# Kernel tuning notes

Measured on AMD Instinct MI355X. Metric: run time of the kernel, lower is better.

Reference implementation:

```python
import jax, jax.numpy as jnp
import numpy as np

B, L, D, N = 8, 512, 768, 64
H = 4 * D  # projection-layer expansion (create_projection_layer: d -> 4d -> out)


def _mlp(x, W1, b1, W2, b2):
    # Linear -> ReLU -> (Dropout, identity in eval) -> Linear
    return jax.nn.relu(x @ W1 + b1) @ W2 + b2


def setup_inputs() -> dict:
    key = jax.random.key(0)
    ks = jax.random.split(key, 18)
    s = 0.02
    inp = {
        "h": jax.random.normal(ks[0], (B, L, D), dtype=jnp.float32),
        "span_idx": jax.random.randint(ks[1], (B, N, 2), 0, L, dtype=jnp.int64),
        # project_start: D -> 4D -> D
        "Ws1": jax.random.normal(ks[2], (D, H), dtype=jnp.float32) * s,
        "bs1": jnp.zeros((H,), jnp.float32),
        "Ws2": jax.random.normal(ks[3], (H, D), dtype=jnp.float32) * s,
        "bs2": jnp.zeros((D,), jnp.float32),
        # project_end: D -> 4D -> D
        "We1": jax.random.normal(ks[4], (D, H), dtype=jnp.float32) * s,
        "be1": jnp.zeros((H,), jnp.float32),
        "We2": jax.random.normal(ks[5], (H, D), dtype=jnp.float32) * s,
        "be2": jnp.zeros((D,), jnp.float32),
        # span_marker.out_project: 2D -> 8D -> D (in=2D so hidden=4*2D? No: create_projection_layer(hidden*2,...)->Linear(2D,4*... ) uses 2D->8D? Faithful: Linear(in, in*4)->Linear(in*4,out) => 2D->8D->D
        "Wo1": jax.random.normal(ks[6], (2 * D, 8 * D), dtype=jnp.float32) * s,
        "bo1": jnp.zeros((8 * D,), jnp.float32),
        "Wo2": jax.random.normal(ks[7], (8 * D, D), dtype=jnp.float32) * s,
        "bo2": jnp.zeros((D,), jnp.float32),
        # rel out_project: 2D -> 8D -> D
        "Wr1": jax.random.normal(ks[8], (2 * D, 8 * D), dtype=jnp.float32) * s,
        "br1": jnp.zeros((8 * D,), jnp.float32),
        "Wr2": jax.random.normal(ks[9], (8 * D, D), dtype=jnp.float32) * s,
        "br2": jnp.zeros((D,), jnp.float32),
    }
    return inp


def reference(h, span_idx, Ws1, bs1, Ws2, bs2, We1, be1, We2, be2,
              Wo1, bo1, Wo2, bo2, Wr1, br1, Wr2, br2):
    Bn, Ln, Dn = h.shape
    Nn = span_idx.shape[1]
    batch_ix = jnp.arange(Bn)[:, None]  # [B,1]

    start_rep = _mlp(h, Ws1, bs1, Ws2, bs2)  # [B,L,D]
    end_rep = _mlp(h, We1, be1, We2, be2)    # [B,L,D]

    # extract_elements: gather span start/end token reps
    start_span = start_rep[batch_ix, span_idx[:, :, 0]]  # [B,N,D]
    end_span = end_rep[batch_ix, span_idx[:, :, 1]]      # [B,N,D]

    cat = jax.nn.relu(jnp.concatenate([start_span, end_span], axis=-1))  # [B,N,2D]
    entity_reps = _mlp(cat, Wo1, bo1, Wo2, bo2)  # [B,N,D]

    # all off-diagonal ordered pairs (i, j), i != j, row-major (matches torch mask)
    ii, jj = np.meshgrid(np.arange(Nn), np.arange(Nn), indexing="ij")
    m = ii != jj
    idx_i = jnp.asarray(ii[m])  # [N*(N-1)]
    idx_j = jnp.asarray(jj[m])

    pairs = jnp.concatenate(
        [entity_reps[:, idx_i], entity_reps[:, idx_j]], axis=-1
    )  # [B, N*(N-1), 2D]

    return _mlp(pairs, Wr1, br1, Wr2, br2)  # [B, N*(N-1), D]
```

## Files before the change

kernel.cpp:

```cpp
#include <hip/hip_runtime.h>

typedef unsigned short u16;
typedef __attribute__((ext_vector_type(8))) short short8;
typedef __attribute__((ext_vector_type(4))) short short4v;
typedef __attribute__((ext_vector_type(4))) float f32x4;

#define DEVI static __device__ __forceinline__

DEVI u16 f2bf(float f) {
  unsigned u = __builtin_bit_cast(unsigned, f);
  u += 0x7FFFu + ((u >> 16) & 1u);
  return (u16)(u >> 16);
}

DEVI float bf2f(u16 x) {
  unsigned u = ((unsigned)x) << 16;
  return __builtin_bit_cast(float, u);
}

DEVI unsigned cvtpk(float lo, float hi) {
  unsigned r;
  asm("v_cvt_pk_bf16_f32 %0, %1, %2" : "=v"(r) : "v"(lo), "v"(hi));
  return r;
}

DEVI void glds16(const void* g, void* l) {
  __builtin_amdgcn_global_load_lds(
      (const __attribute__((address_space(1))) unsigned*)g,
      (__attribute__((address_space(3))) unsigned*)l, 16, 0, 0);
}

struct TSeg { const float* W; u16* WT; int K, N, tstart; };
struct TDesc { TSeg s[8]; };

__global__ void k_transpose_all(TDesc d) {
  __shared__ __align__(16) float t[64][68];
  int bx = blockIdx.x;
  int si = 0;
#pragma unroll
  for (int k = 1; k < 8; ++k) si = (bx >= d.s[k].tstart) ? k : si;
  const float* W = d.s[si].W;
  u16* WT = d.s[si].WT;
  int K = d.s[si].K, N = d.s[si].N;
  int local = bx - d.s[si].tstart;
  int tpr = N >> 6;
  int n0 = (local % tpr) << 6;
  int k0 = (local / tpr) << 6;
  int tx = threadIdx.x;
  int ty = threadIdx.y;
#pragma unroll
  for (int r = 0; r < 4; ++r) {
    float4 v = *(const float4*)(W + (size_t)(k0 + ty * 4 + r) * N + n0 + tx * 4);
    *(float4*)&t[ty * 4 + r][tx * 4] = v;
  }
  __syncthreads();
#pragma unroll
  for (int r = 0; r < 4; ++r) {
    int nr = ty * 4 + r;
    short4v o;
    o[0] = (short)f2bf(t[tx * 4 + 0][nr]);
    o[1] = (short)f2bf(t[tx * 4 + 1][nr]);
    o[2] = (short)f2bf(t[tx * 4 + 2][nr]);
    o[3] = (short)f2bf(t[tx * 4 + 3][nr]);
    *(short4v*)(WT + (size_t)(n0 + nr) * K + k0 + tx * 4) = o;
  }
}

__global__ void k_gather(const float* __restrict__ h,
                         const int* __restrict__ span,
                         u16* __restrict__ xs, u16* __restrict__ xe) {
  int row = blockIdx.x;
  int b = row >> 6;
  int s = span[row * 2 + 0];
  int e = span[row * 2 + 1];
  const float* hs = h + ((size_t)b * 512 + s) * 768;
  const float* he = h + ((size_t)b * 512 + e) * 768;
  for (int d = threadIdx.x; d < 768; d += 256) {
    xs[(size_t)row * 768 + d] = f2bf(hs[d]);
    xe[(size_t)row * 768 + d] = f2bf(he[d]);
  }
}

__global__ __launch_bounds__(256)
void k_gemm(const u16* __restrict__ A0, const u16* __restrict__ A1, int lda,
            const u16* __restrict__ B0, const u16* __restrict__ B1, int ldb,
            const float* __restrict__ bias0, const float* __restrict__ bias1,
            void* __restrict__ C0, void* __restrict__ C1, int ldc,
            int kLen, int mtiles, int nsplit, int flags) {
  __shared__ __align__(16) u16 As[128 * 64];
  __shared__ __align__(16) u16 Bs[128 * 64];
  int z = blockIdx.z;
  int g = z / nsplit, c = z - g * nsplit;
  const u16* A = (g ? A1 : A0) + c * kLen;
  const u16* BT = (g ? B1 : B0) + c * kLen;
  const float* bias = g ? bias1 : bias0;
  void* C = g ? C1 : C0;

  int tid = threadIdx.x;
  int lane = tid & 63;
  int wave = tid >> 6;
  int wr = (wave >> 1) * 64, wc = (wave & 1) * 64;
  int bx = blockIdx.x;
  int m0 = (bx % mtiles) * 128;
  int n0 = (bx / mtiles) * 128;
  const int lr = lane & 15, hi = lane >> 4;

  f32x4 acc[4][4] = {};

  for (int k0 = 0; k0 < kLen; k0 += 64) {
#pragma unroll
    for (int it = 0; it < 4; ++it) {
      int s = it * 256 + tid;
      int row = s >> 3, gg = s & 7;
      int gc = (gg ^ (row & 7)) * 8;
      glds16(A + (size_t)(m0 + row) * lda + k0 + gc, (char*)As + s * 16);
      glds16(BT + (size_t)(n0 + row) * ldb + k0 + gc, (char*)Bs + s * 16);
    }
    __syncthreads();
#pragma unroll
    for (int kk = 0; kk < 2; ++kk) {
      short8 af[4], bf[4];
      int gk = kk * 4 + hi;
#pragma unroll
      for (int m = 0; m < 4; ++m) {
        int row = wr + m * 16 + lr;
        af[m] = *(const short8*)((const char*)As + row * 128 + ((gk ^ (row & 7)) * 16));
      }
#pragma unroll
      for (int n = 0; n < 4; ++n) {
        int row = wc + n * 16 + lr;
        bf[n] = *(const short8*)((const char*)Bs + row * 128 + ((gk ^ (row & 7)) * 16));
      }
#pragma unroll
      for (int m = 0; m < 4; ++m)
#pragma unroll
        for (int n = 0; n < 4; ++n)
          acc[m][n] = __builtin_amdgcn_mfma_f32_16x16x32_bf16(af[m], bf[n], acc[m][n], 0, 0, 0);
    }
    __syncthreads();
  }

  if (flags & 4) {
    float* P = (float*)C + (size_t)c * (mtiles * 128) * ldc;
#pragma unroll
    for (int n = 0; n < 4; ++n) {
      int col = n0 + wc + n * 16 + lr;
#pragma unroll
      for (int m = 0; m < 4; ++m)
#pragma unroll
        for (int r = 0; r < 4; ++r) {
          int row = m0 + wr + m * 16 + hi * 4 + r;
          P[(size_t)row * ldc + col] = acc[m][n][r];
        }
    }
  } else {
    bool relu = flags & 1;
#pragma unroll
    for (int n = 0; n < 4; ++n) {
      int col = n0 + wc + n * 16 + lr;
      float bv = bias ? bias[col] : 0.f;
#pragma unroll
      for (int m = 0; m < 4; ++m)
#pragma unroll
        for (int r = 0; r < 4; ++r) {
          int row = m0 + wr + m * 16 + hi * 4 + r;
          float v = acc[m][n][r] + bv;
          if (relu) v = fmaxf(v, 0.f);
          ((u16*)C)[(size_t)row * ldc + col] = f2bf(v);
        }
    }
  }
}

__global__ void k_fin_cat(const float* __restrict__ Ps, const float* __restrict__ Pe,
                          const float* __restrict__ b0, const float* __restrict__ b1,
                          u16* __restrict__ cat) {
  int t = blockIdx.x * 256 + threadIdx.x;
  int row = t / 384;
  int c4 = (t - row * 384) * 4;
  const float* P = Ps;
  const float* bias = b0;
  int lc = c4;
  if (c4 >= 768) { P = Pe; bias = b1; lc = c4 - 768; }
  f32x4 s = {};
#pragma unroll
  for (int ch = 0; ch < 4; ++ch)
    s += *(const f32x4*)(P + ((size_t)ch * 512 + row) * 768 + lc);
#pragma unroll
  for (int e = 0; e < 4; ++e)
    cat[(size_t)row * 1536 + c4 + e] = f2bf(fmaxf(s[e] + bias[lc + e], 0.f));
}

__global__ void k_fin_ent(const float* __restrict__ Po,
                          const float* __restrict__ bias,
                          u16* __restrict__ ent) {
  int t = blockIdx.x * 256 + threadIdx.x;
  int row = t / 192;
  int c4 = (t - row * 192) * 4;
  f32x4 s = {};
#pragma unroll
  for (int ch = 0; ch < 8; ++ch)
    s += *(const f32x4*)(Po + ((size_t)ch * 512 + row) * 768 + c4);
#pragma unroll
  for (int e = 0; e < 4; ++e)
    ent[(size_t)row * 768 + c4 + e] = f2bf(s[e] + bias[c4 + e]);
}

__global__ __launch_bounds__(512, 4)
void k_pair_gemm(const u16* __restrict__ U, const u16* __restrict__ V,
                 const u16* __restrict__ Wr2T,
                 const float* __restrict__ br2,
                 float* __restrict__ out) {
  __shared__ __align__(16) u16 As[128 * 64];
  __shared__ __align__(16) u16 Bs[2][256 * 64];
  int tid = threadIdx.x;
  int lane = tid & 63;
  int wave = tid >> 6;
  int wr = (wave >> 2) * 64;
  int wc = (wave & 3) * 64;
  const int lr = lane & 15, hi = lane >> 4;

  int nwg = gridDim.x;
  int orig = blockIdx.x;
  int xcd = orig & 7, rem = nwg & 7, qn = nwg >> 3;
  int wgid = (xcd < rem ? xcd * (qn + 1) : rem * (qn + 1) + (xcd - rem) * qn) + (orig >> 3);
  int mt = wgid % 252;
  int nt = wgid / 252;
  int m0 = mt * 128, n0 = nt * 256;

  int r = tid >> 2, q = tid & 3;
  int mrow = m0 + r;
  int b = mrow / 4032;
  int p = mrow - b * 4032;
  int i = p / 63;
  int j0 = p - i * 63;
  int j = j0 + (j0 >= i ? 1 : 0);
  const u16* uR = U + (size_t)(b * 64 + i) * 6144 + q * 16;
  const u16* vR = V + (size_t)(b * 64 + j) * 6144 + q * 16;
  char* aw0 = (char*)As + r * 128 + (((q * 2 + 0) ^ (r & 7)) * 16);
  char* aw1 = (char*)As + r * 128 + (((q * 2 + 1) ^ (r & 7)) * 16);

  f32x4 acc[4][4] = {};

  auto stageB = [&](int t, int buf) {
#pragma unroll
    for (int it = 0; it < 4; ++it) {
      int s = it * 512 + tid;
      int row = s >> 3, g = s & 7;
      int gc = (g ^ (row & 7)) * 8;
      glds16(Wr2T + (size_t)(n0 + row) * 6144 + t * 64 + gc,
             (char*)Bs[buf] + s * 16);
    }
  };

  stageB(0, 0);
  short8 ua = *(const short8*)(uR);
  short8 ub = *(const short8*)(uR + 8);
  short8 vva = *(const short8*)(vR);
  short8 vvb = *(const short8*)(vR + 8);

  for (int t = 0; t < 96; ++t) {
    unsigned w0[4], w1[4];
#pragma unroll
    for (int e = 0; e < 4; ++e) {
      float a0 = fmaxf(bf2f((u16)ua[2 * e])     + bf2f((u16)vva[2 * e]), 0.f);
      float a1 = fmaxf(bf2f((u16)ua[2 * e + 1]) + bf2f((u16)vva[2 * e + 1]), 0.f);
      w0[e] = cvtpk(a0, a1);
      float b0 = fmaxf(bf2f((u16)ub[2 * e])     + bf2f((u16)vvb[2 * e]), 0.f);
      float b1 = fmaxf(bf2f((u16)ub[2 * e + 1]) + bf2f((u16)vvb[2 * e + 1]), 0.f);
      w1[e] = cvtpk(b0, b1);
    }
    __syncthreads();
    *(uint4*)aw0 = *(uint4*)w0;
    *(uint4*)aw1 = *(uint4*)w1;
    if (t + 1 < 96) {
      ua  = *(const short8*)(uR + (t + 1) * 64);
      ub  = *(const short8*)(uR + (t + 1) * 64 + 8);
      vva = *(const short8*)(vR + (t + 1) * 64);
      vvb = *(const short8*)(vR + (t + 1) * 64 + 8);
      stageB(t + 1, (t + 1) & 1);
    }
    asm volatile("s_waitcnt lgkmcnt(0)\n\ts_barrier" ::: "memory");
    __builtin_amdgcn_sched_barrier(0);

    const u16* Bc = Bs[t & 1];
#pragma unroll
    for (int kk = 0; kk < 2; ++kk) {
      short8 af[4], bf[4];
      int gk = kk * 4 + hi;
#pragma unroll
      for (int m = 0; m < 4; ++m) {
        int row = wr + m * 16 + lr;
        af[m] = *(const short8*)((const char*)As + row * 128 + ((gk ^ (row & 7)) * 16));
      }
#pragma unroll
      for (int n = 0; n < 4; ++n) {
        int row = wc + n * 16 + lr;
        bf[n] = *(const short8*)((const char*)Bc + row * 128 + ((gk ^ (row & 7)) * 16));
      }
#pragma unroll
      for (int m = 0; m < 4; ++m)
#pragma unroll
        for (int n = 0; n < 4; ++n)
          acc[m][n] = __builtin_amdgcn_mfma_f32_16x16x32_bf16(af[m], bf[n], acc[m][n], 0, 0, 0);
    }
  }

#pragma unroll
  for (int n = 0; n < 4; ++n) {
    int col = n0 + wc + n * 16 + lr;
    float bv = br2[col];
#pragma unroll
    for (int m = 0; m < 4; ++m)
#pragma unroll
      for (int rg = 0; rg < 4; ++rg) {
        int row = m0 + wr + m * 16 + hi * 4 + rg;
        out[(size_t)row * 768 + col] = acc[m][n][rg] + bv;
      }
  }
}

constexpr size_t OFF_Ws1T = 0;
constexpr size_t OFF_Ws2T = OFF_Ws1T + (size_t)3072 * 768 * 2;
constexpr size_t OFF_We1T = OFF_Ws2T + (size_t)768 * 3072 * 2;
constexpr size_t OFF_We2T = OFF_We1T + (size_t)3072 * 768 * 2;
constexpr size_t OFF_Wo1T = OFF_We2T + (size_t)768 * 3072 * 2;
constexpr size_t OFF_Wo2T = OFF_Wo1T + (size_t)6144 * 1536 * 2;
constexpr size_t OFF_Wr1T = OFF_Wo2T + (size_t)768 * 6144 * 2;
constexpr size_t OFF_Wr2T = OFF_Wr1T + (size_t)6144 * 1536 * 2;
constexpr size_t OFF_XS   = OFF_Wr2T + (size_t)768 * 6144 * 2;
constexpr size_t OFF_XE   = OFF_XS + (size_t)512 * 768 * 2;
constexpr size_t OFF_HS1  = OFF_XE + (size_t)512 * 768 * 2;
constexpr size_t OFF_HE1  = OFF_HS1 + (size_t)512 * 3072 * 2;
constexpr size_t OFF_CAT  = OFF_HE1 + (size_t)512 * 3072 * 2;
constexpr size_t OFF_ENTH = OFF_CAT + (size_t)512 * 1536 * 2;
constexpr size_t OFF_ENT  = OFF_ENTH + (size_t)512 * 6144 * 2;
constexpr size_t OFF_U    = OFF_ENT + (size_t)512 * 768 * 2;
constexpr size_t OFF_V    = OFF_U + (size_t)512 * 6144 * 2;
constexpr size_t OFF_PS   = OFF_V + (size_t)512 * 6144 * 2;
constexpr size_t OFF_PE   = OFF_PS + (size_t)4 * 512 * 768 * 4;
constexpr size_t OFF_PO   = OFF_PS;

extern "C" void kernel_launch(void* const* d_in, const int* in_sizes, int n_in,
                              void* d_out, int out_size, void* d_ws, size_t ws_size,
                              hipStream_t stream) {
  const float* h = (const float*)d_in[0];
  const int* span = (const int*)d_in[1];
  const float* Ws1 = (const float*)d_in[2];
  const float* bs1 = (const float*)d_in[3];
  const float* Ws2 = (const float*)d_in[4];
  const float* bs2 = (const float*)d_in[5];
  const float* We1 = (const float*)d_in[6];
  const float* be1 = (const float*)d_in[7];
  const float* We2 = (const float*)d_in[8];
  const float* be2 = (const float*)d_in[9];
  const float* Wo1 = (const float*)d_in[10];
  const float* bo1 = (const float*)d_in[11];
  const float* Wo2 = (const float*)d_in[12];
  const float* bo2 = (const float*)d_in[13];
  const float* Wr1 = (const float*)d_in[14];
  const float* br1 = (const float*)d_in[15];
  const float* Wr2 = (const float*)d_in[16];
  const float* br2 = (const float*)d_in[17];

  char* ws = (char*)d_ws;
  u16* Ws1T = (u16*)(ws + OFF_Ws1T);
  u16* Ws2T = (u16*)(ws + OFF_Ws2T);
  u16* We1T = (u16*)(ws + OFF_We1T);
  u16* We2T = (u16*)(ws + OFF_We2T);
  u16* Wo1T = (u16*)(ws + OFF_Wo1T);
  u16* Wo2T = (u16*)(ws + OFF_Wo2T);
  u16* Wr1T = (u16*)(ws + OFF_Wr1T);
  u16* Wr2T = (u16*)(ws + OFF_Wr2T);
  u16* xs   = (u16*)(ws + OFF_XS);
  u16* xe   = (u16*)(ws + OFF_XE);
  u16* hs1  = (u16*)(ws + OFF_HS1);
  u16* he1  = (u16*)(ws + OFF_HE1);
  u16* cat  = (u16*)(ws + OFF_CAT);
  u16* enth = (u16*)(ws + OFF_ENTH);
  u16* ent  = (u16*)(ws + OFF_ENT);
  u16* Ub   = (u16*)(ws + OFF_U);
  u16* Vb   = (u16*)(ws + OFF_V);
  float* Ps = (float*)(ws + OFF_PS);
  float* Pe = (float*)(ws + OFF_PE);
  float* Po = (float*)(ws + OFF_PO);

  TDesc td;
  td.s[0] = {Ws1, Ws1T,  768, 3072,    0};
  td.s[1] = {Ws2, Ws2T, 3072,  768,  576};
  td.s[2] = {We1, We1T,  768, 3072, 1152};
  td.s[3] = {We2, We2T, 3072,  768, 1728};
  td.s[4] = {Wo1, Wo1T, 1536, 6144, 2304};
  td.s[5] = {Wo2, Wo2T, 6144,  768, 4608};
  td.s[6] = {Wr1, Wr1T, 1536, 6144, 5760};
  td.s[7] = {Wr2, Wr2T, 6144,  768, 8064};
  k_transpose_all<<<9216, dim3(16, 16), 0, stream>>>(td);

  k_gather<<<512, 256, 0, stream>>>(h, span, xs, xe);

  k_gemm<<<dim3(96, 1, 2), 256, 0, stream>>>(xs, xe, 768, Ws1T, We1T, 768,
      bs1, be1, hs1, he1, 3072, 768, 4, 1, 1 | 2);
  k_gemm<<<dim3(24, 1, 8), 256, 0, stream>>>(hs1, he1, 3072, Ws2T, We2T, 3072,
      nullptr, nullptr, Ps, Pe, 768, 768, 4, 4, 4);
  k_fin_cat<<<768, 256, 0, stream>>>(Ps, Pe, bs2, be2, cat);
  k_gemm<<<dim3(192, 1, 1), 256, 0, stream>>>(cat, cat, 1536, Wo1T, Wo1T, 1536,
      bo1, bo1, enth, enth, 6144, 1536, 4, 1, 1 | 2);
  k_gemm<<<dim3(24, 1, 8), 256, 0, stream>>>(enth, enth, 6144, Wo2T, Wo2T, 6144,
      nullptr, nullptr, Po, Po, 768, 768, 4, 8, 4);
  k_fin_ent<<<384, 256, 0, stream>>>(Po, bo2, ent);
  k_gemm<<<dim3(192, 1, 2), 256, 0, stream>>>(ent, ent, 768, Wr1T, Wr1T + 768, 1536,
      br1, nullptr, Ub, Vb, 6144, 768, 4, 1, 2);
  k_pair_gemm<<<252 * 3, 512, 0, stream>>>(Ub, Vb, Wr2T, br2, (float*)d_out);
}
```

Baseline: 478.6 us.

## Retile pair GEMM to 256x192 with double-buffered A and ping-pong MFMA phases

Changes the final pair-relation GEMM tile from 128x256 to 256x192, so the grid shrinks from 756 to 504 workgroups. The fused relu(U+V) A tile is now double-buffered, and each k-step is split into barrier-separated phases that interleave LDS reads, the next B-tile prefetch and A production with MFMA bursts raised in priority via s_setprio. The aim is to overlap global/LDS traffic with matrix math and to improve operand reuse per wave. The cost is higher LDS use and register pressure (launch bounds lowered to 2 blocks per SM), many more barriers per iteration, and a simplified XCD mapping that assumes exactly 504 blocks.

```diff
diff --git a/kernel.cpp b/kernel.cpp
--- a/kernel.cpp
+++ b/kernel.cpp
@@ -206,45 +206,39 @@
     ent[(size_t)row * 768 + c4 + e] = f2bf(s[e] + bias[c4 + e]);
 }
 
-__global__ __launch_bounds__(512, 4)
+__global__ __launch_bounds__(512, 2)
 void k_pair_gemm(const u16* __restrict__ U, const u16* __restrict__ V,
                  const u16* __restrict__ Wr2T,
                  const float* __restrict__ br2,
                  float* __restrict__ out) {
-  __shared__ __align__(16) u16 As[128 * 64];
-  __shared__ __align__(16) u16 Bs[2][256 * 64];
+  __shared__ __align__(16) u16 As[2][256 * 64];
+  __shared__ __align__(16) u16 Bs[2][192 * 64];
   int tid = threadIdx.x;
   int lane = tid & 63;
   int wave = tid >> 6;
-  int wr = (wave >> 2) * 64;
-  int wc = (wave & 3) * 64;
+  int wr = (wave >> 2) * 128;
+  int wc = (wave & 3) * 48;
   const int lr = lane & 15, hi = lane >> 4;
 
-  int nwg = gridDim.x;
   int orig = blockIdx.x;
-  int xcd = orig & 7, rem = nwg & 7, qn = nwg >> 3;
-  int wgid = (xcd < rem ? xcd * (qn + 1) : rem * (qn + 1) + (xcd - rem) * qn) + (orig >> 3);
-  int mt = wgid % 252;
-  int nt = wgid / 252;
-  int m0 = mt * 128, n0 = nt * 256;
-
-  int r = tid >> 2, q = tid & 3;
+  int wgid = (orig & 7) * 63 + (orig >> 3);
+  int mt = wgid % 126;
+  int nt = wgid / 126;
+  int m0 = mt * 256, n0 = nt * 192;
+
+  int r = tid >> 1, q = tid & 1;
   int mrow = m0 + r;
   int b = mrow / 4032;
   int p = mrow - b * 4032;
   int i = p / 63;
   int j0 = p - i * 63;
   int j = j0 + (j0 >= i ? 1 : 0);
-  const u16* uR = U + (size_t)(b * 64 + i) * 6144 + q * 16;
-  const u16* vR = V + (size_t)(b * 64 + j) * 6144 + q * 16;
-  char* aw0 = (char*)As + r * 128 + (((q * 2 + 0) ^ (r & 7)) * 16);
-  char* aw1 = (char*)As + r * 128 + (((q * 2 + 1) ^ (r & 7)) * 16);
-
-  f32x4 acc[4][4] = {};
+  const u16* uR = U + (size_t)(b * 64 + i) * 6144 + q * 32;
+  const u16* vR = V + (size_t)(b * 64 + j) * 6144 + q * 32;
 
   auto stageB = [&](int t, int buf) {
 #pragma unroll
-    for (int it = 0; it < 4; ++it) {
+    for (int it = 0; it < 3; ++it) {
       int s = it * 512 + tid;
       int row = s >> 3, g = s & 7;
       int gc = (g ^ (row & 7)) * 8;
@@ -253,69 +247,132 @@
     }
   };
 
-  stageB(0, 0);
-  short8 ua = *(const short8*)(uR);
-  short8 ub = *(const short8*)(uR + 8);
-  short8 vva = *(const short8*)(vR);
-  short8 vvb = *(const short8*)(vR + 8);
+  f32x4 accL[4][3] = {};
+  f32x4 accH[4][3] = {};
+
+  {
+    short8 uu[4], vv[4];
+#pragma unroll
+    for (int g = 0; g < 4; ++g) {
+      uu[g] = *(const short8*)(uR + g * 8);
+      vv[g] = *(const short8*)(vR + g * 8);
+    }
+    char* ab = (char*)As[0] + r * 128;
+#pragma unroll
+    for (int g = 0; g < 4; ++g) {
+      unsigned w[4];
+#pragma unroll
+      for (int e = 0; e < 4; ++e)
+        w[e] = cvtpk(fmaxf(bf2f((u16)uu[g][2 * e]) + bf2f((u16)vv[g][2 * e]), 0.f),
+                     fmaxf(bf2f((u16)uu[g][2 * e + 1]) + bf2f((u16)vv[g][2 * e + 1]), 0.f));
+      *(uint4*)(ab + (((q * 4 + g) ^ (r & 7)) * 16)) = *(uint4*)w;
+    }
+    stageB(0, 0);
+  }
+  __syncthreads();
 
   for (int t = 0; t < 96; ++t) {
-    unsigned w0[4], w1[4];
-#pragma unroll
-    for (int e = 0; e < 4; ++e) {
-      float a0 = fmaxf(bf2f((u16)ua[2 * e])     + bf2f((u16)vva[2 * e]), 0.f);
-      float a1 = fmaxf(bf2f((u16)ua[2 * e + 1]) + bf2f((u16)vva[2 * e + 1]), 0.f);
-      w0[e] = cvtpk(a0, a1);
-      float b0 = fmaxf(bf2f((u16)ub[2 * e])     + bf2f((u16)vvb[2 * e]), 0.f);
-      float b1 = fmaxf(bf2f((u16)ub[2 * e + 1]) + bf2f((u16)vvb[2 * e + 1]), 0.f);
-      w1[e] = cvtpk(b0, b1);
-    }
+    const u16* Ac = As[t & 1];
+    const u16* Bc = Bs[t & 1];
+    bool pf = (t + 1 < 96);
+    int gk0 = hi, gk1 = 4 + hi;
+
+    auto rdA = [&](int m, int gk) -> short8 {
+      int row = wr + m * 16 + lr;
+      return *(const short8*)((const char*)Ac + row * 128 + ((gk ^ (row & 7)) * 16));
+    };
+    auto rdB = [&](int n, int gk) -> short8 {
+      int row = wc + n * 16 + lr;
+      return *(const short8*)((const char*)Bc + row * 128 + ((gk ^ (row & 7)) * 16));
+    };
+
+    short8 uu[4], vv[4];
+    short8 bfr[3], af[4];
+
+    if (pf) {
+      const u16* up = uR + (size_t)(t + 1) * 64;
+      const u16* vp = vR + (size_t)(t + 1) * 64;
+#pragma unroll
+      for (int g = 0; g < 4; ++g) {
+        uu[g] = *(const short8*)(up + g * 8);
+        vv[g] = *(const short8*)(vp + g * 8);
+      }
+    }
+    bfr[0] = rdB(0, gk0); bfr[1] = rdB(1, gk0); bfr[2] = rdB(2, gk0);
+    af[0] = rdA(0, gk0); af[1] = rdA(1, gk0); af[2] = rdA(2, gk0); af[3] = rdA(3, gk0);
+    asm volatile("s_barrier" ::: "memory");
+    __builtin_amdgcn_sched_barrier(0);
+    __builtin_amdgcn_s_setprio(1);
+#pragma unroll
+    for (int m = 0; m < 4; ++m)
+#pragma unroll
+      for (int n = 0; n < 3; ++n)
+        accL[m][n] = __builtin_amdgcn_mfma_f32_16x16x32_bf16(af[m], bfr[n], accL[m][n], 0, 0, 0);
+    __builtin_amdgcn_s_setprio(0);
+    asm volatile("s_barrier" ::: "memory");
+
+    if (pf) stageB(t + 1, (t + 1) & 1);
+    af[0] = rdA(4, gk0); af[1] = rdA(5, gk0); af[2] = rdA(6, gk0); af[3] = rdA(7, gk0);
+    asm volatile("s_barrier" ::: "memory");
+    __builtin_amdgcn_sched_barrier(0);
+    __builtin_amdgcn_s_setprio(1);
+#pragma unroll
+    for (int m = 0; m < 4; ++m)
+#pragma unroll
+      for (int n = 0; n < 3; ++n)
+        accH[m][n] = __builtin_amdgcn_mfma_f32_16x16x32_bf16(af[m], bfr[n], accH[m][n], 0, 0, 0);
+    __builtin_amdgcn_s_setprio(0);
+    asm volatile("s_barrier" ::: "memory");
+
+    if (pf) {
+      char* ab = (char*)As[(t + 1) & 1] + r * 128;
+#pragma unroll
+      for (int g = 0; g < 4; ++g) {
+        unsigned w[4];
+#pragma unroll
+        for (int e = 0; e < 4; ++e)
+          w[e] = cvtpk(fmaxf(bf2f((u16)uu[g][2 * e]) + bf2f((u16)vv[g][2 * e]), 0.f),
+                       fmaxf(bf2f((u16)uu[g][2 * e + 1]) + bf2f((u16)vv[g][2 * e + 1]), 0.f));
+        *(uint4*)(ab + (((q * 4 + g) ^ (r & 7)) * 16)) = *(uint4*)w;
+      }
+    }
+    bfr[0] = rdB(0, gk1); bfr[1] = rdB(1, gk1); bfr[2] = rdB(2, gk1);
+    af[0] = rdA(0, gk1); af[1] = rdA(1, gk1); af[2] = rdA(2, gk1); af[3] = rdA(3, gk1);
+    asm volatile("s_barrier" ::: "memory");
+    __builtin_amdgcn_sched_barrier(0);
+    __builtin_amdgcn_s_setprio(1);
+#pragma unroll
+    for (int m = 0; m < 4; ++m)
+#pragma unroll
+      for (int n = 0; n < 3; ++n)
+        accL[m][n] = __builtin_amdgcn_mfma_f32_16x16x32_bf16(af[m], bfr[n], accL[m][n], 0, 0, 0);
+    __builtin_amdgcn_s_setprio(0);
+    asm volatile("s_barrier" ::: "memory");
+
+    af[0] = rdA(4, gk1); af[1] = rdA(5, gk1); af[2] = rdA(6, gk1); af[3] = rdA(7, gk1);
+    asm volatile("s_barrier" ::: "memory");
+    __builtin_amdgcn_sched_barrier(0);
+    __builtin_amdgcn_s_setprio(1);
+#pragma unroll
+    for (int m = 0; m < 4; ++m)
+#pragma unroll
+      for (int n = 0; n < 3; ++n)
+        accH[m][n] = __builtin_amdgcn_mfma_f32_16x16x32_bf16(af[m], bfr[n], accH[m][n], 0, 0, 0);
+    __builtin_amdgcn_s_setprio(0);
     __syncthreads();
-    *(uint4*)aw0 = *(uint4*)w0;
-    *(uint4*)aw1 = *(uint4*)w1;
-    if (t + 1 < 96) {
-      ua  = *(const short8*)(uR + (t + 1) * 64);
-      ub  = *(const short8*)(uR + (t + 1) * 64 + 8);
-      vva = *(const short8*)(vR + (t + 1) * 64);
-      vvb = *(const short8*)(vR + (t + 1) * 64 + 8);
-      stageB(t + 1, (t + 1) & 1);
-    }
-    asm volatile("s_waitcnt lgkmcnt(0)\n\ts_barrier" ::: "memory");
-    __builtin_amdgcn_sched_barrier(0);
-
-    const u16* Bc = Bs[t & 1];
-#pragma unroll
-    for (int kk = 0; kk < 2; ++kk) {
-      short8 af[4], bf[4];
-      int gk = kk * 4 + hi;
-#pragma unroll
-      for (int m = 0; m < 4; ++m) {
-        int row = wr + m * 16 + lr;
-        af[m] = *(const short8*)((const char*)As + row * 128 + ((gk ^ (row & 7)) * 16));
-      }
-#pragma unroll
-      for (int n = 0; n < 4; ++n) {
-        int row = wc + n * 16 + lr;
-        bf[n] = *(const short8*)((const char*)Bc + row * 128 + ((gk ^ (row & 7)) * 16));
-      }
-#pragma unroll
-      for (int m = 0; m < 4; ++m)
-#pragma unroll
-        for (int n = 0; n < 4; ++n)
-          acc[m][n] = __builtin_amdgcn_mfma_f32_16x16x32_bf16(af[m], bf[n], acc[m][n], 0, 0, 0);
-    }
-  }
-
-#pragma unroll
-  for (int n = 0; n < 4; ++n) {
+  }
+
+#pragma unroll
+  for (int n = 0; n < 3; ++n) {
     int col = n0 + wc + n * 16 + lr;
     float bv = br2[col];
 #pragma unroll
     for (int m = 0; m < 4; ++m)
 #pragma unroll
       for (int rg = 0; rg < 4; ++rg) {
-        int row = m0 + wr + m * 16 + hi * 4 + rg;
-        out[(size_t)row * 768 + col] = acc[m][n][rg] + bv;
+        int rowL = m0 + wr + m * 16 + hi * 4 + rg;
+        out[(size_t)rowL * 768 + col] = accL[m][n][rg] + bv;
+        out[(size_t)(rowL + 64) * 768 + col] = accH[m][n][rg] + bv;
       }
   }
 }
@@ -410,5 +467,5 @@
   k_fin_ent<<<384, 256, 0, stream>>>(Po, bo2, ent);
   k_gemm<<<dim3(192, 1, 2), 256, 0, stream>>>(ent, ent, 768, Wr1T, Wr1T + 768, 1536,
       br1, nullptr, Ub, Vb, 6144, 768, 4, 1, 2);
-  k_pair_gemm<<<252 * 3, 512, 0, stream>>>(Ub, Vb, Wr2T, br2, (float*)d_out);
-}
+  k_pair_gemm<<<504, 512, 0, stream>>>(Ub, Vb, Wr2T, br2, (float*)d_out);
+}
```

After: 604.8 us. 1.26x slower.
